# Kernel tuning notes

Measured on AMD Instinct MI355X. Metric: run time of the kernel, lower is better.

## Reference

```python
import jax, jax.numpy as jnp
import numpy as np
import math

B, L, D, H = 8, 1024, 512, 8
HD = D // H


def _proj(x, W, b):
    # torch nn.Linear: y = x @ W.T + b ; then split heads -> (B, H, L, HD)
    bsz, slen, _ = x.shape
    y = x @ W.T + b
    return y.reshape(bsz, slen, H, HD).transpose(0, 2, 1, 3)


def _forward(query, key, value, rel, l1, l2, timestamp, mask, Wq, bq, Wk, bk, Wv, bv):
    bsz, slen, _ = query.shape
    q = _proj(query, Wq, bq)
    k = _proj(key, Wk, bk)
    v = _proj(value, Wv, bv)
    m = mask[:, None, :, :]  # (B,1,L,L), True = masked

    scores = jnp.einsum('bhqd,bhkd->bhqk', q, k) / math.sqrt(HD)
    scores = jnp.where(m, jnp.float32(-1e32), scores)
    prob_attn = jax.nn.softmax(scores, axis=-1)  # (B,H,L,L)

    # rel / timestamp broadcast over heads (original repeats explicitly)
    rel_attn = jax.nn.softmax(jnp.where(m, jnp.float32(-1e5), rel[:, None, :, :]), axis=-1)
    ts = jnp.exp(-jnp.abs(timestamp))
    time_attn = jax.nn.softmax(jnp.where(m, jnp.float32(-1e5), ts[:, None, :, :]), axis=-1)

    # zero out the first query row of each attention map (cat with pad_zero)
    prob_attn = prob_attn.at[:, :, 0, :].set(0.0)
    rel_attn = rel_attn.at[:, :, 0, :].set(0.0)
    time_attn = time_attn.at[:, :, 0, :].set(0.0)

    p = (1.0 - l1) * prob_attn + l1 * rel_attn
    p = (1.0 - l2) * p + l2 * time_attn  # (B,H,L,L) after broadcast

    out = jnp.einsum('bhqk,bhkd->bhqd', p, v)
    out = out.transpose(0, 2, 1, 3).reshape(bsz, slen, D)
    return out, p


def setup_inputs() -> dict:
    key0 = jax.random.key(0)
    ks = jax.random.split(key0, 10)
    s = 1.0 / math.sqrt(D)  # ~ torch Linear init scale
    causal = ~jnp.tril(jnp.ones((L, L), dtype=bool))  # True above diagonal = masked
    return {
        'query': jax.random.normal(ks[0], (B, L, D), jnp.float32),
        'key': jax.random.normal(ks[1], (B, L, D), jnp.float32),
        'value': jax.random.normal(ks[2], (B, L, D), jnp.float32),
        'rel': jax.random.normal(ks[3], (B, L, L), jnp.float32),
        'l1': jnp.float32(0.3),
        'l2': jnp.float32(0.2),
        'timestamp': jax.random.uniform(ks[4], (B, L, L), jnp.float32) * 10.0,
        'mask': jnp.broadcast_to(causal, (B, L, L)),
        'Wq': jax.random.normal(ks[5], (D, D), jnp.float32) * s,
        'bq': jnp.zeros((D,), jnp.float32),
        'Wk': jax.random.normal(ks[6], (D, D), jnp.float32) * s,
        'bk': jnp.zeros((D,), jnp.float32),
        'Wv': jax.random.normal(ks[7], (D, D), jnp.float32) * s,
        'bv': jnp.zeros((D,), jnp.float32),
    }


def reference(query, key, value, rel, l1, l2, timestamp, mask, Wq, bq, Wk, bk, Wv, bv):
    return _forward(query, key, value, rel, l1, l2, timestamp, mask, Wq, bq, Wk, bk, Wv, bv)
```

## Files before the change

kernel.cpp:

```cpp
#include <hip/hip_runtime.h>
#include <hip/hip_bf16.h>
#include <stdint.h>

#define B_ 8
#define L_ 1024
#define D_ 512
#define H_ 8
#define HD_ 64

typedef float f32x4 __attribute__((ext_vector_type(4)));
typedef short s16x8 __attribute__((ext_vector_type(8)));
typedef short s16x4 __attribute__((ext_vector_type(4)));

static __device__ __forceinline__ unsigned short f2bf_bits(float f) {
  union { float f; uint32_t u; } v; v.f = f;
  return (unsigned short)((v.u + 0x7FFFu + ((v.u >> 16) & 1u)) >> 16);
}

#define MFMA16(a, b, c) __builtin_amdgcn_mfma_f32_16x16x32_bf16((a), (b), (c), 0, 0, 0)

__global__ __launch_bounds__(256) void cvt_w_kernel(const float* __restrict__ Wq,
                                                    const float* __restrict__ Wk,
                                                    const float* __restrict__ Wv,
                                                    short* __restrict__ Wb) {
  int idx = blockIdx.x * 256 + threadIdx.x;
  int t = idx >> 16;
  int e4 = idx & 65535;
  const float* src = (t == 0) ? Wq : (t == 1) ? Wk : Wv;
  f32x4 v = *(const f32x4*)(src + (size_t)e4 * 4);
  s16x4 o;
  o.x = (short)f2bf_bits(v.x);
  o.y = (short)f2bf_bits(v.y);
  o.z = (short)f2bf_bits(v.z);
  o.w = (short)f2bf_bits(v.w);
  *(s16x4*)(Wb + (size_t)t * 262144 + (size_t)e4 * 4) = o;
}

__global__ __launch_bounds__(256) void proj_kernel(
    const float* __restrict__ Xq, const float* __restrict__ Xk, const float* __restrict__ Xv,
    const short* __restrict__ Wb,
    const float* __restrict__ bq, const float* __restrict__ bk, const float* __restrict__ bv,
    short* __restrict__ qo, short* __restrict__ ko, short* __restrict__ vo) {
  const int t = blockIdx.z;
  const float* __restrict__ X = (t == 0) ? Xq : (t == 1) ? Xk : Xv;
  const short* __restrict__ W = Wb + (size_t)t * 262144;
  const float* __restrict__ bias = (t == 0) ? bq : (t == 1) ? bk : bv;

  const int m0 = blockIdx.x * 64;
  const int wv = threadIdx.x >> 6;
  const int n0 = blockIdx.y * 256 + wv * 64;
  const int lane = threadIdx.x & 63;
  const int lr = lane & 15, lg = lane >> 4;

  f32x4 acc[4][4] = {};

  for (int k0 = 0; k0 < 512; k0 += 32) {
    s16x8 a[4], b[4];
#pragma unroll
    for (int i = 0; i < 4; i++) {
      const float* ap = X + (size_t)(m0 + i * 16 + lr) * 512 + k0 + lg * 8;
      f32x4 x0 = *(const f32x4*)ap;
      f32x4 x1 = *(const f32x4*)(ap + 4);
      s16x8 av;
#pragma unroll
      for (int j = 0; j < 4; j++) {
        av[j]     = (short)f2bf_bits(x0[j]);
        av[4 + j] = (short)f2bf_bits(x1[j]);
      }
      a[i] = av;
      b[i] = *(const s16x8*)(W + (size_t)(n0 + i * 16 + lr) * 512 + k0 + lg * 8);
    }
#pragma unroll
    for (int i = 0; i < 4; i++)
#pragma unroll
      for (int j = 0; j < 4; j++)
        acc[i][j] = MFMA16(a[i], b[j], acc[i][j]);
  }

#pragma unroll
  for (int i = 0; i < 4; i++) {
    int row0 = m0 + i * 16 + lg * 4;
#pragma unroll
    for (int j = 0; j < 4; j++) {
      int col = n0 + j * 16 + lr;
      float bs = bias[col];
      int h = col >> 6, hd = col & 63;
      if (t < 2) {
        short* dst = (t == 0) ? qo : ko;
#pragma unroll
        for (int r = 0; r < 4; r++) {
          int m = row0 + r;
          int bb = m >> 10, l = m & 1023;
          dst[(((size_t)(bb * 8 + h)) * 1024 + l) * 64 + hd] =
              (short)f2bf_bits(acc[i][j][r] + bs);
        }
      } else {
        int m = row0;
        int bb = m >> 10, l = m & 1023;
        s16x4 o;
#pragma unroll
        for (int r = 0; r < 4; r++) o[r] = (short)f2bf_bits(acc[i][j][r] + bs);
        *(s16x4*)(vo + ((size_t)(bb * 8 + h) * 64 + hd) * 1024 + l) = o;
      }
    }
  }
}

__global__ __launch_bounds__(256) void rcomb_kernel(const float* __restrict__ rel,
                                                    const float* __restrict__ ts,
                                                    const float* __restrict__ l1p,
                                                    const float* __restrict__ l2p,
                                                    float* __restrict__ rc) {
  int bq = blockIdx.x;
  int q = bq & 1023;
  int tid = threadIdx.x;
  const float* relrow = rel + (size_t)bq * 1024;
  const float* tsrow = ts + (size_t)bq * 1024;
  float* outrow = rc + (size_t)bq * 1024;

  int k0 = tid * 4;
  f32x4 rv = *(const f32x4*)(relrow + k0);
  f32x4 tv = *(const f32x4*)(tsrow + k0);
  f32x4 e1, e2;
  float s1 = 0.f, s2 = 0.f;
#pragma unroll
  for (int j = 0; j < 4; j++) {
    bool ok = (k0 + j) <= q;
    float a = ok ? __expf(rv[j]) : 0.f;
    float c = ok ? __expf(__expf(-fabsf(tv[j]))) : 0.f;
    e1[j] = a; e2[j] = c;
    s1 += a; s2 += c;
  }
#pragma unroll
  for (int m = 32; m; m >>= 1) {
    s1 += __shfl_xor(s1, m);
    s2 += __shfl_xor(s2, m);
  }
  __shared__ float red[2][4];
  if ((tid & 63) == 0) { red[0][tid >> 6] = s1; red[1][tid >> 6] = s2; }
  __syncthreads();
  s1 = red[0][0] + red[0][1] + red[0][2] + red[0][3];
  s2 = red[1][0] + red[1][1] + red[1][2] + red[1][3];

  float l1 = *l1p, l2 = *l2p;
  float wrel = (1.f - l2) * l1 / s1;
  float wt = l2 / s2;
  f32x4 o;
  if (q == 0) {
    o.x = o.y = o.z = o.w = 0.f;
  } else {
#pragma unroll
    for (int j = 0; j < 4; j++) o[j] = e1[j] * wrel + e2[j] * wt;
  }
  *(f32x4*)(outrow + k0) = o;
}

__global__ __launch_bounds__(256) void attn_kernel(
    const short* __restrict__ Qb, const short* __restrict__ Kb, const short* __restrict__ VTb,
    const float* __restrict__ rc, const float* __restrict__ l1p, const float* __restrict__ l2p,
    float* __restrict__ outp, float* __restrict__ pout) {
  const int bh = blockIdx.y;
  const int b = bh >> 3, h = bh & 7;
  const int w = threadIdx.x >> 6;
  const int lane = threadIdx.x & 63;
  const int lr = lane & 15, lg = lane >> 4;
  const int q0 = blockIdx.x * 64 + w * 16;

  const short* __restrict__ Q = Qb + (size_t)bh * 1024 * 64;
  const short* __restrict__ K = Kb + (size_t)bh * 1024 * 64;
  const short* __restrict__ VT = VTb + (size_t)bh * 64 * 1024;

  __shared__ short plds[4][16][72];

  s16x8 aq0 = *(const s16x8*)(Q + (size_t)(q0 + lr) * 64 + lg * 8);
  s16x8 aq1 = *(const s16x8*)(Q + (size_t)(q0 + lr) * 64 + 32 + lg * 8);

  const float l1v = *l1p, l2v = *l2p;
  const float wprob = (1.f - l2v) * (1.f - l1v);
  const int qmax = q0 + 15;

  float esum[4] = {0.f, 0.f, 0.f, 0.f};
  for (int k0 = 0; k0 <= qmax; k0 += 64) {
#pragma unroll
    for (int n = 0; n < 4; n++) {
      int kb = k0 + n * 16;
      s16x8 b0 = *(const s16x8*)(K + (size_t)(kb + lr) * 64 + lg * 8);
      s16x8 b1 = *(const s16x8*)(K + (size_t)(kb + lr) * 64 + 32 + lg * 8);
      f32x4 s = {};
      s = MFMA16(aq0, b0, s);
      s = MFMA16(aq1, b1, s);
      int key = kb + lr;
#pragma unroll
      for (int r = 0; r < 4; r++) {
        int qq = q0 + lg * 4 + r;
        if (key <= qq) esum[r] += __expf(s[r] * 0.125f);
      }
    }
  }
  float inv[4];
#pragma unroll
  for (int r = 0; r < 4; r++) {
    float e = esum[r];
    e += __shfl_xor(e, 1, 16);
    e += __shfl_xor(e, 2, 16);
    e += __shfl_xor(e, 4, 16);
    e += __shfl_xor(e, 8, 16);
    int qq = q0 + lg * 4 + r;
    inv[r] = (qq == 0) ? 0.f : (wprob / e);
  }

  f32x4 oacc[4] = {};
  float* __restrict__ prow = pout + (size_t)bh * 1024 * 1024;
  const float* __restrict__ rcb = rc + (size_t)b * 1024 * 1024;

  for (int k0 = 0; k0 < 1024; k0 += 64) {
    if (k0 <= qmax) {
#pragma unroll
      for (int n = 0; n < 4; n++) {
        int kb = k0 + n * 16;
        s16x8 b0 = *(const s16x8*)(K + (size_t)(kb + lr) * 64 + lg * 8);
        s16x8 b1 = *(const s16x8*)(K + (size_t)(kb + lr) * 64 + 32 + lg * 8);
        f32x4 s = {};
        s = MFMA16(aq0, b0, s);
        s = MFMA16(aq1, b1, s);
        int key = kb + lr;
#pragma unroll
        for (int r = 0; r < 4; r++) {
          int qq = q0 + lg * 4 + r;
          float pv = 0.f;
          if (key <= qq) {
            float rcv = rcb[(size_t)qq * 1024 + key];
            pv = __expf(s[r] * 0.125f) * inv[r] + rcv;
          }
          prow[(size_t)qq * 1024 + key] = pv;
          plds[w][lg * 4 + r][n * 16 + lr] = (short)f2bf_bits(pv);
        }
      }
#pragma unroll
      for (int sub = 0; sub < 2; sub++) {
        s16x8 pa = *(const s16x8*)(&plds[w][lr][sub * 32 + lg * 8]);
#pragma unroll
        for (int dblk = 0; dblk < 4; dblk++) {
          s16x8 bvf = *(const s16x8*)(VT + (size_t)(dblk * 16 + lr) * 1024 + k0 + sub * 32 + lg * 8);
          oacc[dblk] = MFMA16(pa, bvf, oacc[dblk]);
        }
      }
    } else {
#pragma unroll
      for (int n = 0; n < 4; n++) {
        int key = k0 + n * 16 + lr;
#pragma unroll
        for (int r = 0; r < 4; r++) {
          int qq = q0 + lg * 4 + r;
          prow[(size_t)qq * 1024 + key] = 0.f;
        }
      }
    }
  }

  float* __restrict__ orow = outp + (size_t)b * 1024 * 512 + h * 64;
#pragma unroll
  for (int dblk = 0; dblk < 4; dblk++)
#pragma unroll
    for (int r = 0; r < 4; r++) {
      int qq = q0 + lg * 4 + r;
      orow[(size_t)qq * 512 + dblk * 16 + lr] = oacc[dblk][r];
    }
}

extern "C" void kernel_launch(void* const* d_in, const int* in_sizes, int n_in,
                              void* d_out, int out_size, void* d_ws, size_t ws_size,
                              hipStream_t stream) {
  const float* query = (const float*)d_in[0];
  const float* key   = (const float*)d_in[1];
  const float* value = (const float*)d_in[2];
  const float* rel   = (const float*)d_in[3];
  const float* l1p   = (const float*)d_in[4];
  const float* l2p   = (const float*)d_in[5];
  const float* tsp   = (const float*)d_in[6];
  const float* Wq = (const float*)d_in[8];
  const float* bq = (const float*)d_in[9];
  const float* Wk = (const float*)d_in[10];
  const float* bk = (const float*)d_in[11];
  const float* Wv = (const float*)d_in[12];
  const float* bv = (const float*)d_in[13];

  char* ws = (char*)d_ws;
  short* wb  = (short*)(ws);
  short* qb  = (short*)(ws + (2u << 20));
  short* kb  = (short*)(ws + (10u << 20));
  short* vtb = (short*)(ws + (18u << 20));
  float* rcb = (float*)(ws + (26u << 20));

  float* outp = (float*)d_out;
  float* pout = outp + (size_t)B_ * L_ * D_;

  cvt_w_kernel<<<768, 256, 0, stream>>>(Wq, Wk, Wv, wb);
  proj_kernel<<<dim3(128, 2, 3), 256, 0, stream>>>(query, key, value, wb,
                                                   bq, bk, bv, qb, kb, vtb);
  rcomb_kernel<<<B_ * L_, 256, 0, stream>>>(rel, tsp, l1p, l2p, rcb);
  attn_kernel<<<dim3(L_ / 64, B_ * H_), 256, 0, stream>>>(qb, kb, vtb, rcb,
                                                          l1p, l2p, outp, pout);
}
```

Measured before the change: 679.8 us.

## Transpose score MFMA for row-contiguous P stores, pre-convert inputs, swizzle blocks

The attention kernel swaps MFMA operand order (K as A, Q as B) so each lane owns one query row and four consecutive keys. This lets the P matrix and the rc reads use 16-byte vector accesses, and the LDS writes of P become 8-byte vectors. The row-sum reduction shrinks to two cross-lane shuffles. Input activations are now converted to bf16 in a combined conversion kernel rather than inside the projection loop, and the attention grid is flattened with a block-index swizzle. The costs are an extra global round-trip for the bf16 activations and the rc buffer aliasing the xb workspace region, which relies on the launch order.

```diff
diff --git a/kernel.cpp b/kernel.cpp
--- a/kernel.cpp
+++ b/kernel.cpp
@@ -19,30 +19,41 @@
 
 #define MFMA16(a, b, c) __builtin_amdgcn_mfma_f32_16x16x32_bf16((a), (b), (c), 0, 0, 0)
 
-__global__ __launch_bounds__(256) void cvt_w_kernel(const float* __restrict__ Wq,
-                                                    const float* __restrict__ Wk,
-                                                    const float* __restrict__ Wv,
-                                                    short* __restrict__ Wb) {
+__global__ __launch_bounds__(256) void cvt_all_kernel(
+    const float* __restrict__ Wq, const float* __restrict__ Wk, const float* __restrict__ Wv,
+    const float* __restrict__ Xq, const float* __restrict__ Xk, const float* __restrict__ Xv,
+    short* __restrict__ wb, short* __restrict__ xb) {
   int idx = blockIdx.x * 256 + threadIdx.x;
-  int t = idx >> 16;
-  int e4 = idx & 65535;
-  const float* src = (t == 0) ? Wq : (t == 1) ? Wk : Wv;
+  const float* __restrict__ src;
+  short* __restrict__ dst;
+  int e4;
+  if (idx < 196608) {
+    int t = idx >> 16;
+    e4 = idx & 65535;
+    src = (t == 0) ? Wq : (t == 1) ? Wk : Wv;
+    dst = wb + (size_t)t * 262144;
+  } else {
+    int xi = idx - 196608;
+    int t = xi >> 20;
+    e4 = xi & 1048575;
+    src = (t == 0) ? Xq : (t == 1) ? Xk : Xv;
+    dst = xb + (size_t)t * 4194304;
+  }
   f32x4 v = *(const f32x4*)(src + (size_t)e4 * 4);
   s16x4 o;
   o.x = (short)f2bf_bits(v.x);
   o.y = (short)f2bf_bits(v.y);
   o.z = (short)f2bf_bits(v.z);
   o.w = (short)f2bf_bits(v.w);
-  *(s16x4*)(Wb + (size_t)t * 262144 + (size_t)e4 * 4) = o;
+  *(s16x4*)(dst + (size_t)e4 * 4) = o;
 }
 
 __global__ __launch_bounds__(256) void proj_kernel(
-    const float* __restrict__ Xq, const float* __restrict__ Xk, const float* __restrict__ Xv,
-    const short* __restrict__ Wb,
+    const short* __restrict__ Xb, const short* __restrict__ Wb,
     const float* __restrict__ bq, const float* __restrict__ bk, const float* __restrict__ bv,
     short* __restrict__ qo, short* __restrict__ ko, short* __restrict__ vo) {
   const int t = blockIdx.z;
-  const float* __restrict__ X = (t == 0) ? Xq : (t == 1) ? Xk : Xv;
+  const short* __restrict__ X = Xb + (size_t)t * 4194304;
   const short* __restrict__ W = Wb + (size_t)t * 262144;
   const float* __restrict__ bias = (t == 0) ? bq : (t == 1) ? bk : bv;
 
@@ -58,16 +69,7 @@
     s16x8 a[4], b[4];
 #pragma unroll
     for (int i = 0; i < 4; i++) {
-      const float* ap = X + (size_t)(m0 + i * 16 + lr) * 512 + k0 + lg * 8;
-      f32x4 x0 = *(const f32x4*)ap;
-      f32x4 x1 = *(const f32x4*)(ap + 4);
-      s16x8 av;
-#pragma unroll
-      for (int j = 0; j < 4; j++) {
-        av[j]     = (short)f2bf_bits(x0[j]);
-        av[4 + j] = (short)f2bf_bits(x1[j]);
-      }
-      a[i] = av;
+      a[i] = *(const s16x8*)(X + (size_t)(m0 + i * 16 + lr) * 512 + k0 + lg * 8);
       b[i] = *(const s16x8*)(W + (size_t)(n0 + i * 16 + lr) * 512 + k0 + lg * 8);
     }
 #pragma unroll
@@ -159,82 +161,74 @@
     const short* __restrict__ Qb, const short* __restrict__ Kb, const short* __restrict__ VTb,
     const float* __restrict__ rc, const float* __restrict__ l1p, const float* __restrict__ l2p,
     float* __restrict__ outp, float* __restrict__ pout) {
-  const int bh = blockIdx.y;
+  int id = blockIdx.x;
+  int sw = ((id & 7) << 7) | (id >> 3);
+  const int bx = sw & 15, bh = sw >> 4;
   const int b = bh >> 3, h = bh & 7;
   const int w = threadIdx.x >> 6;
   const int lane = threadIdx.x & 63;
   const int lr = lane & 15, lg = lane >> 4;
-  const int q0 = blockIdx.x * 64 + w * 16;
-
-  const short* __restrict__ Q = Qb + (size_t)bh * 1024 * 64;
-  const short* __restrict__ K = Kb + (size_t)bh * 1024 * 64;
-  const short* __restrict__ VT = VTb + (size_t)bh * 64 * 1024;
+  const int q0 = bx * 64 + w * 16;
+  const int qq = q0 + lr;
+  const int qmax = q0 + 15;
+
+  const short* __restrict__ Q = Qb + (size_t)bh * 65536;
+  const short* __restrict__ K = Kb + (size_t)bh * 65536;
+  const short* __restrict__ VT = VTb + (size_t)bh * 65536;
 
   __shared__ short plds[4][16][72];
 
-  s16x8 aq0 = *(const s16x8*)(Q + (size_t)(q0 + lr) * 64 + lg * 8);
-  s16x8 aq1 = *(const s16x8*)(Q + (size_t)(q0 + lr) * 64 + 32 + lg * 8);
-
-  const float l1v = *l1p, l2v = *l2p;
-  const float wprob = (1.f - l2v) * (1.f - l1v);
-  const int qmax = q0 + 15;
-
-  float esum[4] = {0.f, 0.f, 0.f, 0.f};
+  s16x8 qf0 = *(const s16x8*)(Q + (size_t)(q0 + lr) * 64 + lg * 8);
+  s16x8 qf1 = *(const s16x8*)(Q + (size_t)(q0 + lr) * 64 + 32 + lg * 8);
+
+  const float wprob = (1.f - *l2p) * (1.f - *l1p);
+
+  float esum = 0.f;
   for (int k0 = 0; k0 <= qmax; k0 += 64) {
 #pragma unroll
     for (int n = 0; n < 4; n++) {
-      int kb = k0 + n * 16;
-      s16x8 b0 = *(const s16x8*)(K + (size_t)(kb + lr) * 64 + lg * 8);
-      s16x8 b1 = *(const s16x8*)(K + (size_t)(kb + lr) * 64 + 32 + lg * 8);
+      int kb_ = k0 + n * 16;
+      s16x8 kf0 = *(const s16x8*)(K + (size_t)(kb_ + lr) * 64 + lg * 8);
+      s16x8 kf1 = *(const s16x8*)(K + (size_t)(kb_ + lr) * 64 + 32 + lg * 8);
       f32x4 s = {};
-      s = MFMA16(aq0, b0, s);
-      s = MFMA16(aq1, b1, s);
-      int key = kb + lr;
-#pragma unroll
-      for (int r = 0; r < 4; r++) {
-        int qq = q0 + lg * 4 + r;
-        if (key <= qq) esum[r] += __expf(s[r] * 0.125f);
-      }
-    }
-  }
-  float inv[4];
-#pragma unroll
-  for (int r = 0; r < 4; r++) {
-    float e = esum[r];
-    e += __shfl_xor(e, 1, 16);
-    e += __shfl_xor(e, 2, 16);
-    e += __shfl_xor(e, 4, 16);
-    e += __shfl_xor(e, 8, 16);
-    int qq = q0 + lg * 4 + r;
-    inv[r] = (qq == 0) ? 0.f : (wprob / e);
-  }
+      s = MFMA16(kf0, qf0, s);
+      s = MFMA16(kf1, qf1, s);
+      int key = kb_ + lg * 4;
+#pragma unroll
+      for (int r = 0; r < 4; r++)
+        if (key + r <= qq) esum += __expf(s[r] * 0.125f);
+    }
+  }
+  esum += __shfl_xor(esum, 16);
+  esum += __shfl_xor(esum, 32);
+  const float inv = (qq == 0) ? 0.f : (wprob / esum);
 
   f32x4 oacc[4] = {};
-  float* __restrict__ prow = pout + (size_t)bh * 1024 * 1024;
-  const float* __restrict__ rcb = rc + (size_t)b * 1024 * 1024;
+  float* __restrict__ pq = pout + (size_t)bh * 1048576 + (size_t)qq * 1024;
+  const float* __restrict__ rcrow = rc + (size_t)b * 1048576 + (size_t)qq * 1024;
 
   for (int k0 = 0; k0 < 1024; k0 += 64) {
     if (k0 <= qmax) {
 #pragma unroll
       for (int n = 0; n < 4; n++) {
-        int kb = k0 + n * 16;
-        s16x8 b0 = *(const s16x8*)(K + (size_t)(kb + lr) * 64 + lg * 8);
-        s16x8 b1 = *(const s16x8*)(K + (size_t)(kb + lr) * 64 + 32 + lg * 8);
+        int kb_ = k0 + n * 16;
+        int key = kb_ + lg * 4;
+        f32x4 rcv = *(const f32x4*)(rcrow + key);
+        s16x8 kf0 = *(const s16x8*)(K + (size_t)(kb_ + lr) * 64 + lg * 8);
+        s16x8 kf1 = *(const s16x8*)(K + (size_t)(kb_ + lr) * 64 + 32 + lg * 8);
         f32x4 s = {};
-        s = MFMA16(aq0, b0, s);
-        s = MFMA16(aq1, b1, s);
-        int key = kb + lr;
+        s = MFMA16(kf0, qf0, s);
+        s = MFMA16(kf1, qf1, s);
+        f32x4 pv;
+        s16x4 pb;
 #pragma unroll
         for (int r = 0; r < 4; r++) {
-          int qq = q0 + lg * 4 + r;
-          float pv = 0.f;
-          if (key <= qq) {
-            float rcv = rcb[(size_t)qq * 1024 + key];
-            pv = __expf(s[r] * 0.125f) * inv[r] + rcv;
-          }
-          prow[(size_t)qq * 1024 + key] = pv;
-          plds[w][lg * 4 + r][n * 16 + lr] = (short)f2bf_bits(pv);
+          float val = (key + r <= qq) ? (__expf(s[r] * 0.125f) * inv + rcv[r]) : 0.f;
+          pv[r] = val;
+          pb[r] = (short)f2bf_bits(val);
         }
+        *(f32x4*)(pq + key) = pv;
+        *(s16x4*)(&plds[w][lr][n * 16 + lg * 4]) = pb;
       }
 #pragma unroll
       for (int sub = 0; sub < 2; sub++) {
@@ -246,26 +240,19 @@
         }
       }
     } else {
-#pragma unroll
-      for (int n = 0; n < 4; n++) {
-        int key = k0 + n * 16 + lr;
-#pragma unroll
-        for (int r = 0; r < 4; r++) {
-          int qq = q0 + lg * 4 + r;
-          prow[(size_t)qq * 1024 + key] = 0.f;
-        }
-      }
-    }
-  }
-
-  float* __restrict__ orow = outp + (size_t)b * 1024 * 512 + h * 64;
+      f32x4 z = {};
+#pragma unroll
+      for (int n = 0; n < 4; n++)
+        *(f32x4*)(pq + k0 + n * 16 + lg * 4) = z;
+    }
+  }
+
+  float* __restrict__ orow = outp + (size_t)b * 524288 + h * 64;
 #pragma unroll
   for (int dblk = 0; dblk < 4; dblk++)
 #pragma unroll
-    for (int r = 0; r < 4; r++) {
-      int qq = q0 + lg * 4 + r;
-      orow[(size_t)qq * 512 + dblk * 16 + lr] = oacc[dblk][r];
-    }
+    for (int r = 0; r < 4; r++)
+      orow[(size_t)(q0 + lg * 4 + r) * 512 + dblk * 16 + lr] = oacc[dblk][r];
 }
 
 extern "C" void kernel_launch(void* const* d_in, const int* in_sizes, int n_in,
@@ -287,18 +274,17 @@
 
   char* ws = (char*)d_ws;
   short* wb  = (short*)(ws);
-  short* qb  = (short*)(ws + (2u << 20));
-  short* kb  = (short*)(ws + (10u << 20));
-  short* vtb = (short*)(ws + (18u << 20));
-  float* rcb = (float*)(ws + (26u << 20));
+  short* xb  = (short*)(ws + (2u << 20));
+  float* rcb = (float*)(ws + (2u << 20));
+  short* qb  = (short*)(ws + (34u << 20));
+  short* kb  = (short*)(ws + (42u << 20));
+  short* vtb = (short*)(ws + (50u << 20));
 
   float* outp = (float*)d_out;
   float* pout = outp + (size_t)B_ * L_ * D_;
 
-  cvt_w_kernel<<<768, 256, 0, stream>>>(Wq, Wk, Wv, wb);
-  proj_kernel<<<dim3(128, 2, 3), 256, 0, stream>>>(query, key, value, wb,
-                                                   bq, bk, bv, qb, kb, vtb);
+  cvt_all_kernel<<<13056, 256, 0, stream>>>(Wq, Wk, Wv, query, key, value, wb, xb);
+  proj_kernel<<<dim3(128, 2, 3), 256, 0, stream>>>(xb, wb, bq, bk, bv, qb, kb, vtb);
   rcomb_kernel<<<B_ * L_, 256, 0, stream>>>(rel, tsp, l1p, l2p, rcb);
-  attn_kernel<<<dim3(L_ / 64, B_ * H_), 256, 0, stream>>>(qb, kb, vtb, rcb,
-                                                          l1p, l2p, outp, pout);
-}
+  attn_kernel<<<1024, 256, 0, stream>>>(qb, kb, vtb, rcb, l1p, l2p, outp, pout);
+}
```

Result: faster. 595.1 us (-12.5%).
